# Performance work log

Measured on AMD Instinct MI355X. Metric: run time of the kernel, lower is better.

Reference implementation:

```python
import jax, jax.numpy as jnp
import numpy as np

B, T, IN, H, OUT = 4096, 512, 4, 64, 1


def setup_inputs() -> dict:
    key = jax.random.key(0)
    ks = jax.random.split(key, 12)
    s_in = 1.0 / np.sqrt(H)
    u = lambda k, shape: jax.random.uniform(k, shape, jnp.float32, -s_in, s_in)
    return {
        "x": jax.random.normal(ks[0], (B, T, IN), jnp.float32),
        "W_ih0": u(ks[1], (4 * H, IN)),
        "W_hh0": u(ks[2], (4 * H, H)),
        "b_ih0": u(ks[3], (4 * H,)),
        "b_hh0": u(ks[4], (4 * H,)),
        "W_ih1": u(ks[5], (4 * H, H)),
        "W_hh1": u(ks[6], (4 * H, H)),
        "b_ih1": u(ks[7], (4 * H,)),
        "b_hh1": u(ks[8], (4 * H,)),
        "W_fc": u(ks[9], (OUT, H)),
        "b_fc": u(ks[10], (OUT,)),
    }


def _lstm_layer(x_seq, W_ih, W_hh, b_ih, b_hh):
    # x_seq: [B, T, D]. PyTorch gate order: i, f, g, o.
    # Precompute input projection for all timesteps (one big GEMM).
    x_proj = jnp.einsum("btd,gd->btg", x_seq, W_ih) + b_ih + b_hh  # [B, T, 4H]
    x_proj = jnp.swapaxes(x_proj, 0, 1)  # [T, B, 4H]
    Bsz = x_seq.shape[0]
    h0 = jnp.zeros((Bsz, W_hh.shape[1]), x_seq.dtype)
    c0 = jnp.zeros_like(h0)

    def step(carry, xp):
        h, c = carry
        gates = xp + h @ W_hh.T  # [B, 4H]
        i, f, g, o = jnp.split(gates, 4, axis=-1)
        i = jax.nn.sigmoid(i)
        f = jax.nn.sigmoid(f)
        g = jnp.tanh(g)
        o = jax.nn.sigmoid(o)
        c_new = f * c + i * g
        h_new = o * jnp.tanh(c_new)
        return (h_new, c_new), h_new

    (hT, cT), h_seq = jax.lax.scan(step, (h0, c0), x_proj)
    return jnp.swapaxes(h_seq, 0, 1), hT  # [B, T, H], [B, H]


def reference(x, W_ih0, W_hh0, b_ih0, b_hh0, W_ih1, W_hh1, b_ih1, b_hh1, W_fc, b_fc):
    h1_seq, _ = _lstm_layer(x, W_ih0, W_hh0, b_ih0, b_hh0)
    _, h2_last = _lstm_layer(h1_seq, W_ih1, W_hh1, b_ih1, b_hh1)
    return h2_last @ W_fc.T + b_fc  # [B, 1]
```

## Files before the change

kernel.cpp:

```cpp
#include <hip/hip_runtime.h>

#define TSEQ 512
#define NTH  512

typedef __attribute__((ext_vector_type(8))) _Float16 half8;
typedef __attribute__((ext_vector_type(4))) float f32x4;
typedef __attribute__((ext_vector_type(4))) unsigned int u32x4;

__device__ __forceinline__ unsigned packF16x2(float a, float b) {
    _Float16 ha = (_Float16)a, hb = (_Float16)b;
    unsigned short ua = __builtin_bit_cast(unsigned short, ha);
    unsigned short ub = __builtin_bit_cast(unsigned short, hb);
    return (unsigned)ua | ((unsigned)ub << 16);
}
__device__ __forceinline__ half8 packA16s(const float w8[8], float s) {
    u32x4 W = { packF16x2(w8[0]*s, w8[1]*s), packF16x2(w8[2]*s, w8[3]*s),
                packF16x2(w8[4]*s, w8[5]*s), packF16x2(w8[6]*s, w8[7]*s) };
    return __builtin_bit_cast(half8, W);
}

#define MFMA(a, b, c) __builtin_amdgcn_mfma_f32_16x16x32_f16((a), (b), (c), 0, 0, 0)
#define LD128H(p) __builtin_bit_cast(half8, *(const u32x4*)(p))

__device__ __forceinline__ float act_fused(float ai, float af, float ag, float ao, float* c) {
    const float L2E2 = 2.88539008177792681472f;
    float ei = __builtin_amdgcn_exp2f(ai);
    float ef = __builtin_amdgcn_exp2f(af);
    float eg = __builtin_amdgcn_exp2f(ag);
    float eo = __builtin_amdgcn_exp2f(ao);
    float sf = __builtin_amdgcn_rcpf(1.0f + ef);
    float ig = (eg - 1.0f) * __builtin_amdgcn_rcpf((1.0f + ei) * (eg + 1.0f));
    float cn = fmaf(*c, sf, ig);
    *c = cn;
    float ec = __builtin_amdgcn_exp2f(cn * L2E2);
    return (ec - 1.0f) * __builtin_amdgcn_rcpf((1.0f + eo) * (ec + 1.0f));
}

__global__ __launch_bounds__(NTH, 1)
void lstm2_mfma(const float* __restrict__ x,
                const float* __restrict__ W_ih0, const float* __restrict__ W_hh0,
                const float* __restrict__ b_ih0, const float* __restrict__ b_hh0,
                const float* __restrict__ W_ih1, const float* __restrict__ W_hh1,
                const float* __restrict__ b_ih1, const float* __restrict__ b_hh1,
                const float* __restrict__ W_fc,  const float* __restrict__ b_fc,
                float* __restrict__ out)
{
    const int tid  = threadIdx.x;
    const int lane = tid & 63;
    const int wv   = tid >> 6;
    const int rl   = lane & 15;
    const int g    = lane >> 4;
    const int b0   = blockIdx.x * 16;

    const float NL2E = -1.44269504088896340736f;
    const float PL2E2 = 2.88539008177792681472f;

    __shared__ unsigned h0P0[512], h0P1[512];
    __shared__ unsigned h1P0[512], h1P1[512];
    __shared__ float fcl[64 * 17];

    for (int i2 = tid; i2 < 512; i2 += NTH) {
        h0P0[i2] = 0u; h0P1[i2] = 0u; h1P0[i2] = 0u; h1P1[i2] = 0u;
    }
    __syncthreads();

    const int offL = rl*32 + (((g + rl) & 7) << 2);
    const int offH = rl*32 + (((4 + g + rl) & 7) << 2);
    const int q0w  = 8*((wv & 3)) + 2*g;
    const int woff = rl*32 + ((((q0w >> 2) + rl) & 7) << 2) + (q0w & 3);

    if (wv < 4) {
        const int w = wv;
        half8 A0[4][2];
        half8 Ax[4];
        f32x4 bias4[4];
        #pragma unroll
        for (int G = 0; G < 4; ++G) {
            const float sc = (G == 2) ? PL2E2 : NL2E;
            const int row = 64*G + 16*w + rl;
            #pragma unroll
            for (int s = 0; s < 2; ++s) {
                float w8[8];
                const float* src = W_hh0 + row*64 + s*32 + g*8;
                #pragma unroll
                for (int e = 0; e < 8; ++e) w8[e] = src[e];
                A0[G][s] = packA16s(w8, sc);
            }
            {
                u32x4 ax = {0u, 0u, 0u, 0u};
                if (g == 0) {
                    ax.x = packF16x2(W_ih0[row*4+0]*sc, W_ih0[row*4+1]*sc);
                    ax.y = packF16x2(W_ih0[row*4+2]*sc, W_ih0[row*4+3]*sc);
                }
                Ax[G] = __builtin_bit_cast(half8, ax);
            }
            const int rb = 64*G + 16*w + 4*g;
            bias4[G].x = (b_ih0[rb+0] + b_hh0[rb+0]) * sc;
            bias4[G].y = (b_ih0[rb+1] + b_hh0[rb+1]) * sc;
            bias4[G].z = (b_ih0[rb+2] + b_hh0[rb+2]) * sc;
            bias4[G].w = (b_ih0[rb+3] + b_hh0[rb+3]) * sc;
        }
        float cst[4] = {0.f, 0.f, 0.f, 0.f};

        f32x4 xf = *(const f32x4*)(x + ((size_t)(b0 + rl) * TSEQ) * 4);
        unsigned bx0 = packF16x2(xf.x, xf.y);
        unsigned bx1 = packF16x2(xf.z, xf.w);

        auto body0 = [&](const unsigned* rP, unsigned* wP, int i) {
            if (i + 1 < TSEQ)
                xf = *(const f32x4*)(x + ((size_t)(b0 + rl) * TSEQ + (i + 1)) * 4);

            half8 B0 = LD128H(rP + offL);
            half8 B1 = LD128H(rP + offH);
            u32x4 tx = {0u, 0u, 0u, 0u};
            if (g == 0) { tx.x = bx0; tx.y = bx1; }
            half8 Bx = __builtin_bit_cast(half8, tx);

            f32x4 acc[4];
            __builtin_amdgcn_s_setprio(1);
            #pragma unroll
            for (int G = 0; G < 4; ++G) acc[G] = MFMA(Ax[G], Bx, bias4[G]);
            #pragma unroll
            for (int G = 0; G < 4; ++G) acc[G] = MFMA(A0[G][0], B0, acc[G]);
            #pragma unroll
            for (int G = 0; G < 4; ++G) acc[G] = MFMA(A0[G][1], B1, acc[G]);
            __builtin_amdgcn_s_setprio(0);

            float hv[4];
            #pragma unroll
            for (int j = 0; j < 4; ++j)
                hv[j] = act_fused(acc[0][j], acc[1][j], acc[2][j], acc[3][j], &cst[j]);

            bx0 = packF16x2(xf.x, xf.y);
            bx1 = packF16x2(xf.z, xf.w);

            *(uint2*)(wP + woff) = make_uint2(packF16x2(hv[0], hv[1]),
                                              packF16x2(hv[2], hv[3]));
        };

        for (int ii = 0; ii < 256; ++ii) {
            body0(h0P0, h0P1, 2*ii);     __syncthreads();
            body0(h0P1, h0P0, 2*ii + 1); __syncthreads();
        }
        __syncthreads();
        __syncthreads();
    } else {
        const int w = wv - 4;
        half8 A1[4][4];
        f32x4 bias4[4];
        #pragma unroll
        for (int G = 0; G < 4; ++G) {
            const float sc = (G == 2) ? PL2E2 : NL2E;
            const int row = 64*G + 16*w + rl;
            #pragma unroll
            for (int s = 0; s < 4; ++s) {
                float w8[8];
                const float* src = (s < 2) ? (W_ih1 + row*64 + s*32 + g*8)
                                           : (W_hh1 + row*64 + (s-2)*32 + g*8);
                #pragma unroll
                for (int e = 0; e < 8; ++e) w8[e] = src[e];
                A1[G][s] = packA16s(w8, sc);
            }
            const int rb = 64*G + 16*w + 4*g;
            bias4[G].x = (b_ih1[rb+0] + b_hh1[rb+0]) * sc;
            bias4[G].y = (b_ih1[rb+1] + b_hh1[rb+1]) * sc;
            bias4[G].z = (b_ih1[rb+2] + b_hh1[rb+2]) * sc;
            bias4[G].w = (b_ih1[rb+3] + b_hh1[rb+3]) * sc;
        }
        float cst[4] = {0.f, 0.f, 0.f, 0.f};
        const int u0 = 16*w + 4*g;

        half8 pB0 = {}, pB1 = {};

        auto body1 = [&](const unsigned* r1P,
                         unsigned* wP,
                         const unsigned* n0P,
                         bool wrFC) {
            half8 B2 = LD128H(r1P + offL);
            half8 B3 = LD128H(r1P + offH);

            f32x4 acc[4];
            __builtin_amdgcn_s_setprio(1);
            #pragma unroll
            for (int G = 0; G < 4; ++G) acc[G] = MFMA(A1[G][0], pB0, bias4[G]);
            #pragma unroll
            for (int G = 0; G < 4; ++G) acc[G] = MFMA(A1[G][1], pB1, acc[G]);
            #pragma unroll
            for (int G = 0; G < 4; ++G) acc[G] = MFMA(A1[G][2], B2, acc[G]);
            #pragma unroll
            for (int G = 0; G < 4; ++G) acc[G] = MFMA(A1[G][3], B3, acc[G]);
            __builtin_amdgcn_s_setprio(0);

            pB0 = LD128H(n0P + offL);
            pB1 = LD128H(n0P + offH);

            float hv[4];
            #pragma unroll
            for (int j = 0; j < 4; ++j)
                hv[j] = act_fused(acc[0][j], acc[1][j], acc[2][j], acc[3][j], &cst[j]);
            *(uint2*)(wP + woff) = make_uint2(packF16x2(hv[0], hv[1]),
                                              packF16x2(hv[2], hv[3]));
            if (wrFC) {
                #pragma unroll
                for (int j = 0; j < 4; ++j) fcl[(u0 + j)*17 + rl] = hv[j];
            }
        };

        __syncthreads();
        pB0 = LD128H(h0P1 + offL);
        pB1 = LD128H(h0P1 + offH);
        __syncthreads();
        for (int ii = 0; ii < 256; ++ii) {
            body1(h1P0, h1P1, h0P0, false);     __syncthreads();
            body1(h1P1, h1P0, h0P1, ii == 255); __syncthreads();
        }
    }

    if (tid < 16) {
        float acc = b_fc[0];
        #pragma unroll 16
        for (int u = 0; u < 64; ++u) acc += fcl[u*17 + tid] * W_fc[u];
        out[b0 + tid] = acc;
    }
}

extern "C" void kernel_launch(void* const* d_in, const int* in_sizes, int n_in,
                              void* d_out, int out_size, void* d_ws, size_t ws_size,
                              hipStream_t stream) {
    const float* x     = (const float*)d_in[0];
    const float* W_ih0 = (const float*)d_in[1];
    const float* W_hh0 = (const float*)d_in[2];
    const float* b_ih0 = (const float*)d_in[3];
    const float* b_hh0 = (const float*)d_in[4];
    const float* W_ih1 = (const float*)d_in[5];
    const float* W_hh1 = (const float*)d_in[6];
    const float* b_ih1 = (const float*)d_in[7];
    const float* b_hh1 = (const float*)d_in[8];
    const float* W_fc  = (const float*)d_in[9];
    const float* b_fc  = (const float*)d_in[10];
    float* out = (float*)d_out;

    dim3 grid(4096 / 16), block(NTH);
    hipLaunchKernelGGL(lstm2_mfma, grid, block, 0, stream,
                       x, W_ih0, W_hh0, b_ih0, b_hh0,
                       W_ih1, W_hh1, b_ih1, b_hh1, W_fc, b_fc, out);
}
```

Measured before the change: 341.7 us.

## Halve batch tile per block and give each wave two hidden-unit tiles

Blocks now handle 8 batch rows with 256 threads (two waves per layer) instead of 16 rows with 512 threads, and the grid doubles. Each wave keeps two 16-row weight tiles per gate and issues twice as many MFMAs per step. The 16 MFMA columns carry duplicated batch rows, and each lane selects the accumulator tile that matches its half. The aim is to cut per-block synchronization scope and spread the recurrence across more blocks. In exchange, MFMA work per batch element doubles, the serial MFMA chain per step gets longer, and register use for weights rises.

```diff
diff --git a/kernel.cpp b/kernel.cpp
--- a/kernel.cpp
+++ b/kernel.cpp
@@ -1,7 +1,8 @@
 #include <hip/hip_runtime.h>
 
 #define TSEQ 512
-#define NTH  512
+#define NTH  256
+#define BT   8
 
 typedef __attribute__((ext_vector_type(8))) _Float16 half8;
 typedef __attribute__((ext_vector_type(4))) float f32x4;
@@ -50,65 +51,68 @@
     const int wv   = tid >> 6;
     const int rl   = lane & 15;
     const int g    = lane >> 4;
-    const int b0   = blockIdx.x * 16;
-
-    const float NL2E = -1.44269504088896340736f;
-    const float PL2E2 = 2.88539008177792681472f;
-
-    __shared__ unsigned h0P0[512], h0P1[512];
-    __shared__ unsigned h1P0[512], h1P1[512];
-    __shared__ float fcl[64 * 17];
-
-    for (int i2 = tid; i2 < 512; i2 += NTH) {
+    const int n    = rl & 7;
+    const int T    = rl >> 3;
+    const int b0   = blockIdx.x * BT;
+    const int w    = wv & 1;
+
+    const float NL2E  = -1.44269504088896340736f;
+    const float PL2E2 =  2.88539008177792681472f;
+
+    __shared__ unsigned h0P0[256], h0P1[256];
+    __shared__ unsigned h1P0[256], h1P1[256];
+    __shared__ float fcl[64 * 9];
+
+    for (int i2 = tid; i2 < 256; i2 += NTH) {
         h0P0[i2] = 0u; h0P1[i2] = 0u; h1P0[i2] = 0u; h1P1[i2] = 0u;
     }
     __syncthreads();
 
-    const int offL = rl*32 + (((g + rl) & 7) << 2);
-    const int offH = rl*32 + (((4 + g + rl) & 7) << 2);
-    const int q0w  = 8*((wv & 3)) + 2*g;
-    const int woff = rl*32 + ((((q0w >> 2) + rl) & 7) << 2) + (q0w & 3);
-
-    if (wv < 4) {
-        const int w = wv;
-        half8 A0[4][2];
-        half8 Ax[4];
-        f32x4 bias4[4];
+    const int offL = n*32 + (((g + n) & 7) << 2);
+    const int offH = n*32 + (((4 + g + n) & 7) << 2);
+    const int q0w  = 16*w + 8*T + 2*g;
+    const int woff = n*32 + ((((q0w >> 2) + n) & 7) << 2) + (q0w & 3);
+
+    if (wv < 2) {
+        half8 A0[4][2][2];
+        half8 Ax[4][2];
+        f32x4 bias4[4][2];
         #pragma unroll
         for (int G = 0; G < 4; ++G) {
             const float sc = (G == 2) ? PL2E2 : NL2E;
-            const int row = 64*G + 16*w + rl;
-            #pragma unroll
-            for (int s = 0; s < 2; ++s) {
-                float w8[8];
-                const float* src = W_hh0 + row*64 + s*32 + g*8;
+            #pragma unroll
+            for (int Tt = 0; Tt < 2; ++Tt) {
+                const int row = 64*G + 32*w + 16*Tt + rl;
                 #pragma unroll
-                for (int e = 0; e < 8; ++e) w8[e] = src[e];
-                A0[G][s] = packA16s(w8, sc);
-            }
-            {
+                for (int s = 0; s < 2; ++s) {
+                    float w8[8];
+                    const float* src = W_hh0 + row*64 + s*32 + g*8;
+                    #pragma unroll
+                    for (int e = 0; e < 8; ++e) w8[e] = src[e];
+                    A0[G][s][Tt] = packA16s(w8, sc);
+                }
                 u32x4 ax = {0u, 0u, 0u, 0u};
                 if (g == 0) {
                     ax.x = packF16x2(W_ih0[row*4+0]*sc, W_ih0[row*4+1]*sc);
                     ax.y = packF16x2(W_ih0[row*4+2]*sc, W_ih0[row*4+3]*sc);
                 }
-                Ax[G] = __builtin_bit_cast(half8, ax);
+                Ax[G][Tt] = __builtin_bit_cast(half8, ax);
+                const int rb = 64*G + 32*w + 16*Tt + 4*g;
+                bias4[G][Tt].x = (b_ih0[rb+0] + b_hh0[rb+0]) * sc;
+                bias4[G][Tt].y = (b_ih0[rb+1] + b_hh0[rb+1]) * sc;
+                bias4[G][Tt].z = (b_ih0[rb+2] + b_hh0[rb+2]) * sc;
+                bias4[G][Tt].w = (b_ih0[rb+3] + b_hh0[rb+3]) * sc;
             }
-            const int rb = 64*G + 16*w + 4*g;
-            bias4[G].x = (b_ih0[rb+0] + b_hh0[rb+0]) * sc;
-            bias4[G].y = (b_ih0[rb+1] + b_hh0[rb+1]) * sc;
-            bias4[G].z = (b_ih0[rb+2] + b_hh0[rb+2]) * sc;
-            bias4[G].w = (b_ih0[rb+3] + b_hh0[rb+3]) * sc;
         }
         float cst[4] = {0.f, 0.f, 0.f, 0.f};
 
-        f32x4 xf = *(const f32x4*)(x + ((size_t)(b0 + rl) * TSEQ) * 4);
+        f32x4 xf = *(const f32x4*)(x + ((size_t)(b0 + n) * TSEQ) * 4);
         unsigned bx0 = packF16x2(xf.x, xf.y);
         unsigned bx1 = packF16x2(xf.z, xf.w);
 
         auto body0 = [&](const unsigned* rP, unsigned* wP, int i) {
             if (i + 1 < TSEQ)
-                xf = *(const f32x4*)(x + ((size_t)(b0 + rl) * TSEQ + (i + 1)) * 4);
+                xf = *(const f32x4*)(x + ((size_t)(b0 + n) * TSEQ + (i + 1)) * 4);
 
             half8 B0 = LD128H(rP + offL);
             half8 B1 = LD128H(rP + offH);
@@ -116,20 +120,30 @@
             if (g == 0) { tx.x = bx0; tx.y = bx1; }
             half8 Bx = __builtin_bit_cast(half8, tx);
 
-            f32x4 acc[4];
+            f32x4 acc[2][4];
             __builtin_amdgcn_s_setprio(1);
             #pragma unroll
-            for (int G = 0; G < 4; ++G) acc[G] = MFMA(Ax[G], Bx, bias4[G]);
-            #pragma unroll
-            for (int G = 0; G < 4; ++G) acc[G] = MFMA(A0[G][0], B0, acc[G]);
-            #pragma unroll
-            for (int G = 0; G < 4; ++G) acc[G] = MFMA(A0[G][1], B1, acc[G]);
+            for (int G = 0; G < 4; ++G) acc[0][G] = MFMA(Ax[G][0], Bx, bias4[G][0]);
+            #pragma unroll
+            for (int G = 0; G < 4; ++G) acc[1][G] = MFMA(Ax[G][1], Bx, bias4[G][1]);
+            #pragma unroll
+            for (int G = 0; G < 4; ++G) acc[0][G] = MFMA(A0[G][0][0], B0, acc[0][G]);
+            #pragma unroll
+            for (int G = 0; G < 4; ++G) acc[1][G] = MFMA(A0[G][0][1], B0, acc[1][G]);
+            #pragma unroll
+            for (int G = 0; G < 4; ++G) acc[0][G] = MFMA(A0[G][1][0], B1, acc[0][G]);
+            #pragma unroll
+            for (int G = 0; G < 4; ++G) acc[1][G] = MFMA(A0[G][1][1], B1, acc[1][G]);
             __builtin_amdgcn_s_setprio(0);
 
+            f32x4 s0 = T ? acc[1][0] : acc[0][0];
+            f32x4 s1 = T ? acc[1][1] : acc[0][1];
+            f32x4 s2 = T ? acc[1][2] : acc[0][2];
+            f32x4 s3 = T ? acc[1][3] : acc[0][3];
             float hv[4];
             #pragma unroll
             for (int j = 0; j < 4; ++j)
-                hv[j] = act_fused(acc[0][j], acc[1][j], acc[2][j], acc[3][j], &cst[j]);
+                hv[j] = act_fused(s0[j], s1[j], s2[j], s3[j], &cst[j]);
 
             bx0 = packF16x2(xf.x, xf.y);
             bx1 = packF16x2(xf.z, xf.w);
@@ -145,64 +159,76 @@
         __syncthreads();
         __syncthreads();
     } else {
-        const int w = wv - 4;
-        half8 A1[4][4];
-        f32x4 bias4[4];
+        half8 A1[4][4][2];
+        f32x4 bias4[4][2];
         #pragma unroll
         for (int G = 0; G < 4; ++G) {
             const float sc = (G == 2) ? PL2E2 : NL2E;
-            const int row = 64*G + 16*w + rl;
-            #pragma unroll
-            for (int s = 0; s < 4; ++s) {
-                float w8[8];
-                const float* src = (s < 2) ? (W_ih1 + row*64 + s*32 + g*8)
-                                           : (W_hh1 + row*64 + (s-2)*32 + g*8);
+            #pragma unroll
+            for (int Tt = 0; Tt < 2; ++Tt) {
+                const int row = 64*G + 32*w + 16*Tt + rl;
                 #pragma unroll
-                for (int e = 0; e < 8; ++e) w8[e] = src[e];
-                A1[G][s] = packA16s(w8, sc);
+                for (int s = 0; s < 4; ++s) {
+                    float w8[8];
+                    const float* src = (s < 2) ? (W_ih1 + row*64 + s*32 + g*8)
+                                               : (W_hh1 + row*64 + (s-2)*32 + g*8);
+                    #pragma unroll
+                    for (int e = 0; e < 8; ++e) w8[e] = src[e];
+                    A1[G][s][Tt] = packA16s(w8, sc);
+                }
+                const int rb = 64*G + 32*w + 16*Tt + 4*g;
+                bias4[G][Tt].x = (b_ih1[rb+0] + b_hh1[rb+0]) * sc;
+                bias4[G][Tt].y = (b_ih1[rb+1] + b_hh1[rb+1]) * sc;
+                bias4[G][Tt].z = (b_ih1[rb+2] + b_hh1[rb+2]) * sc;
+                bias4[G][Tt].w = (b_ih1[rb+3] + b_hh1[rb+3]) * sc;
             }
-            const int rb = 64*G + 16*w + 4*g;
-            bias4[G].x = (b_ih1[rb+0] + b_hh1[rb+0]) * sc;
-            bias4[G].y = (b_ih1[rb+1] + b_hh1[rb+1]) * sc;
-            bias4[G].z = (b_ih1[rb+2] + b_hh1[rb+2]) * sc;
-            bias4[G].w = (b_ih1[rb+3] + b_hh1[rb+3]) * sc;
         }
         float cst[4] = {0.f, 0.f, 0.f, 0.f};
-        const int u0 = 16*w + 4*g;
+        const int u0 = 32*w + 16*T + 4*g;
 
         half8 pB0 = {}, pB1 = {};
 
-        auto body1 = [&](const unsigned* r1P,
-                         unsigned* wP,
-                         const unsigned* n0P,
-                         bool wrFC) {
+        auto body1 = [&](const unsigned* r1P, unsigned* wP,
+                         const unsigned* n0P, bool wrFC) {
             half8 B2 = LD128H(r1P + offL);
             half8 B3 = LD128H(r1P + offH);
 
-            f32x4 acc[4];
+            f32x4 acc[2][4];
             __builtin_amdgcn_s_setprio(1);
             #pragma unroll
-            for (int G = 0; G < 4; ++G) acc[G] = MFMA(A1[G][0], pB0, bias4[G]);
-            #pragma unroll
-            for (int G = 0; G < 4; ++G) acc[G] = MFMA(A1[G][1], pB1, acc[G]);
-            #pragma unroll
-            for (int G = 0; G < 4; ++G) acc[G] = MFMA(A1[G][2], B2, acc[G]);
-            #pragma unroll
-            for (int G = 0; G < 4; ++G) acc[G] = MFMA(A1[G][3], B3, acc[G]);
+            for (int G = 0; G < 4; ++G) acc[0][G] = MFMA(A1[G][0][0], pB0, bias4[G][0]);
+            #pragma unroll
+            for (int G = 0; G < 4; ++G) acc[1][G] = MFMA(A1[G][0][1], pB0, bias4[G][1]);
+            #pragma unroll
+            for (int G = 0; G < 4; ++G) acc[0][G] = MFMA(A1[G][1][0], pB1, acc[0][G]);
+            #pragma unroll
+            for (int G = 0; G < 4; ++G) acc[1][G] = MFMA(A1[G][1][1], pB1, acc[1][G]);
+            #pragma unroll
+            for (int G = 0; G < 4; ++G) acc[0][G] = MFMA(A1[G][2][0], B2, acc[0][G]);
+            #pragma unroll
+            for (int G = 0; G < 4; ++G) acc[1][G] = MFMA(A1[G][2][1], B2, acc[1][G]);
+            #pragma unroll
+            for (int G = 0; G < 4; ++G) acc[0][G] = MFMA(A1[G][3][0], B3, acc[0][G]);
+            #pragma unroll
+            for (int G = 0; G < 4; ++G) acc[1][G] = MFMA(A1[G][3][1], B3, acc[1][G]);
             __builtin_amdgcn_s_setprio(0);
 
             pB0 = LD128H(n0P + offL);
             pB1 = LD128H(n0P + offH);
 
+            f32x4 s0 = T ? acc[1][0] : acc[0][0];
+            f32x4 s1 = T ? acc[1][1] : acc[0][1];
+            f32x4 s2 = T ? acc[1][2] : acc[0][2];
+            f32x4 s3 = T ? acc[1][3] : acc[0][3];
             float hv[4];
             #pragma unroll
             for (int j = 0; j < 4; ++j)
-                hv[j] = act_fused(acc[0][j], acc[1][j], acc[2][j], acc[3][j], &cst[j]);
+                hv[j] = act_fused(s0[j], s1[j], s2[j], s3[j], &cst[j]);
             *(uint2*)(wP + woff) = make_uint2(packF16x2(hv[0], hv[1]),
                                               packF16x2(hv[2], hv[3]));
             if (wrFC) {
                 #pragma unroll
-                for (int j = 0; j < 4; ++j) fcl[(u0 + j)*17 + rl] = hv[j];
+                for (int j = 0; j < 4; ++j) fcl[(u0 + j)*9 + n] = hv[j];
             }
         };
 
@@ -216,10 +242,10 @@
         }
     }
 
-    if (tid < 16) {
+    if (tid < BT) {
         float acc = b_fc[0];
         #pragma unroll 16
-        for (int u = 0; u < 64; ++u) acc += fcl[u*17 + tid] * W_fc[u];
+        for (int u = 0; u < 64; ++u) acc += fcl[u*9 + tid] * W_fc[u];
         out[b0 + tid] = acc;
     }
 }
@@ -240,7 +266,7 @@
     const float* b_fc  = (const float*)d_in[10];
     float* out = (float*)d_out;
 
-    dim3 grid(4096 / 16), block(NTH);
+    dim3 grid(4096 / BT), block(NTH);
     hipLaunchKernelGGL(lstm2_mfma, grid, block, 0, stream,
                        x, W_ih0, W_hh0, b_ih0, b_hh0,
                        W_ih1, W_hh1, b_ih1, b_hh1, W_fc, b_fc, out);
```

Measured after the change: 667.7 us. +95.4%, slower.

## Split each LSTM step into MFMA and activation phases interleaved across layers

Applied to the files above, without the earlier changes.

Each timestep is split into two phases separated by barriers. While layer 0 runs its MFMAs, layer 1 runs its activations, and the reverse in the next phase, so the two wave groups use the matrix and vector units at different times instead of contending. Layer 1 now keeps a single h buffer in shared memory. The cost is twice as many __syncthreads per timestep, which may outweigh the gain from the overlap.

```diff
diff --git a/kernel.cpp b/kernel.cpp
--- a/kernel.cpp
+++ b/kernel.cpp
@@ -52,15 +52,15 @@
     const int g    = lane >> 4;
     const int b0   = blockIdx.x * 16;
 
-    const float NL2E = -1.44269504088896340736f;
-    const float PL2E2 = 2.88539008177792681472f;
+    const float NL2E  = -1.44269504088896340736f;
+    const float PL2E2 =  2.88539008177792681472f;
 
     __shared__ unsigned h0P0[512], h0P1[512];
-    __shared__ unsigned h1P0[512], h1P1[512];
+    __shared__ unsigned h1P[512];
     __shared__ float fcl[64 * 17];
 
     for (int i2 = tid; i2 < 512; i2 += NTH) {
-        h0P0[i2] = 0u; h0P1[i2] = 0u; h1P0[i2] = 0u; h1P1[i2] = 0u;
+        h0P0[i2] = 0u; h0P1[i2] = 0u; h1P[i2] = 0u;
     }
     __syncthreads();
 
@@ -101,22 +101,20 @@
             bias4[G].w = (b_ih0[rb+3] + b_hh0[rb+3]) * sc;
         }
         float cst[4] = {0.f, 0.f, 0.f, 0.f};
+        f32x4 acc[4];
 
         f32x4 xf = *(const f32x4*)(x + ((size_t)(b0 + rl) * TSEQ) * 4);
         unsigned bx0 = packF16x2(xf.x, xf.y);
         unsigned bx1 = packF16x2(xf.z, xf.w);
 
-        auto body0 = [&](const unsigned* rP, unsigned* wP, int i) {
+        auto ph1 = [&](const unsigned* rP, int i) {
             if (i + 1 < TSEQ)
                 xf = *(const f32x4*)(x + ((size_t)(b0 + rl) * TSEQ + (i + 1)) * 4);
-
             half8 B0 = LD128H(rP + offL);
             half8 B1 = LD128H(rP + offH);
             u32x4 tx = {0u, 0u, 0u, 0u};
             if (g == 0) { tx.x = bx0; tx.y = bx1; }
             half8 Bx = __builtin_bit_cast(half8, tx);
-
-            f32x4 acc[4];
             __builtin_amdgcn_s_setprio(1);
             #pragma unroll
             for (int G = 0; G < 4; ++G) acc[G] = MFMA(Ax[G], Bx, bias4[G]);
@@ -125,25 +123,29 @@
             #pragma unroll
             for (int G = 0; G < 4; ++G) acc[G] = MFMA(A0[G][1], B1, acc[G]);
             __builtin_amdgcn_s_setprio(0);
-
+        };
+        auto ph2 = [&](unsigned* wP) {
             float hv[4];
             #pragma unroll
             for (int j = 0; j < 4; ++j)
                 hv[j] = act_fused(acc[0][j], acc[1][j], acc[2][j], acc[3][j], &cst[j]);
-
             bx0 = packF16x2(xf.x, xf.y);
             bx1 = packF16x2(xf.z, xf.w);
-
             *(uint2*)(wP + woff) = make_uint2(packF16x2(hv[0], hv[1]),
                                               packF16x2(hv[2], hv[3]));
         };
 
-        for (int ii = 0; ii < 256; ++ii) {
-            body0(h0P0, h0P1, 2*ii);     __syncthreads();
-            body0(h0P1, h0P0, 2*ii + 1); __syncthreads();
-        }
-        __syncthreads();
-        __syncthreads();
+        for (int ii = 0; ii <= 256; ++ii) {
+            const int i0 = 2*ii, i1 = 2*ii + 1;
+            if (i0 < TSEQ) ph1(h0P0, i0);
+            __syncthreads();
+            if (i0 < TSEQ) ph2(h0P1);
+            __syncthreads();
+            if (i1 < TSEQ) ph1(h0P1, i1);
+            __syncthreads();
+            if (i1 < TSEQ) ph2(h0P0);
+            __syncthreads();
+        }
     } else {
         const int w = wv - 4;
         half8 A1[4][4];
@@ -169,50 +171,54 @@
         }
         float cst[4] = {0.f, 0.f, 0.f, 0.f};
         const int u0 = 16*w + 4*g;
-
+        f32x4 acc[4];
         half8 pB0 = {}, pB1 = {};
 
-        auto body1 = [&](const unsigned* r1P,
-                         unsigned* wP,
-                         const unsigned* n0P,
-                         bool wrFC) {
-            half8 B2 = LD128H(r1P + offL);
-            half8 B3 = LD128H(r1P + offH);
-
-            f32x4 acc[4];
-            __builtin_amdgcn_s_setprio(1);
-            #pragma unroll
-            for (int G = 0; G < 4; ++G) acc[G] = MFMA(A1[G][0], pB0, bias4[G]);
-            #pragma unroll
-            for (int G = 0; G < 4; ++G) acc[G] = MFMA(A1[G][1], pB1, acc[G]);
-            #pragma unroll
-            for (int G = 0; G < 4; ++G) acc[G] = MFMA(A1[G][2], B2, acc[G]);
-            #pragma unroll
-            for (int G = 0; G < 4; ++G) acc[G] = MFMA(A1[G][3], B3, acc[G]);
-            __builtin_amdgcn_s_setprio(0);
-
-            pB0 = LD128H(n0P + offL);
-            pB1 = LD128H(n0P + offH);
-
-            float hv[4];
-            #pragma unroll
-            for (int j = 0; j < 4; ++j)
-                hv[j] = act_fused(acc[0][j], acc[1][j], acc[2][j], acc[3][j], &cst[j]);
-            *(uint2*)(wP + woff) = make_uint2(packF16x2(hv[0], hv[1]),
-                                              packF16x2(hv[2], hv[3]));
-            if (wrFC) {
-                #pragma unroll
-                for (int j = 0; j < 4; ++j) fcl[(u0 + j)*17 + rl] = hv[j];
-            }
-        };
-
-        __syncthreads();
-        pB0 = LD128H(h0P1 + offL);
-        pB1 = LD128H(h0P1 + offH);
-        __syncthreads();
-        for (int ii = 0; ii < 256; ++ii) {
-            body1(h1P0, h1P1, h0P0, false);     __syncthreads();
-            body1(h1P1, h1P0, h0P1, ii == 255); __syncthreads();
+        auto ph1 = [&](const unsigned* n0P, int i) {
+            if (i >= 2) {
+                float hv[4];
+                #pragma unroll
+                for (int j = 0; j < 4; ++j)
+                    hv[j] = act_fused(acc[0][j], acc[1][j], acc[2][j], acc[3][j], &cst[j]);
+                *(uint2*)(h1P + woff) = make_uint2(packF16x2(hv[0], hv[1]),
+                                                   packF16x2(hv[2], hv[3]));
+                if (i == TSEQ + 1) {
+                    #pragma unroll
+                    for (int j = 0; j < 4; ++j) fcl[(u0 + j)*17 + rl] = hv[j];
+                }
+            }
+            if (i >= 1 && i <= TSEQ) {
+                pB0 = LD128H(n0P + offL);
+                pB1 = LD128H(n0P + offH);
+            }
+        };
+        auto ph2 = [&](int i) {
+            if (i >= 1 && i <= TSEQ) {
+                half8 B2 = LD128H(h1P + offL);
+                half8 B3 = LD128H(h1P + offH);
+                __builtin_amdgcn_s_setprio(1);
+                #pragma unroll
+                for (int G = 0; G < 4; ++G) acc[G] = MFMA(A1[G][0], pB0, bias4[G]);
+                #pragma unroll
+                for (int G = 0; G < 4; ++G) acc[G] = MFMA(A1[G][1], pB1, acc[G]);
+                #pragma unroll
+                for (int G = 0; G < 4; ++G) acc[G] = MFMA(A1[G][2], B2, acc[G]);
+                #pragma unroll
+                for (int G = 0; G < 4; ++G) acc[G] = MFMA(A1[G][3], B3, acc[G]);
+                __builtin_amdgcn_s_setprio(0);
+            }
+        };
+
+        for (int ii = 0; ii <= 256; ++ii) {
+            const int i0 = 2*ii, i1 = 2*ii + 1;
+            ph1(h0P0, i0);
+            __syncthreads();
+            ph2(i0);
+            __syncthreads();
+            ph1(h0P1, i1);
+            __syncthreads();
+            ph2(i1);
+            __syncthreads();
         }
     }
 
```

New measurement: 363.2 us. +6.3%, slower.

## Halve batch per block to 8 and split activations across MFMA column halves

Applied to the files above, without the earlier changes.

Each block now handles 8 batch rows instead of 16, which doubles the grid to 512 blocks and allows two blocks per CU via launch bounds. The 16 MFMA columns now hold 8 batch rows duplicated across two halves. Each lane evaluates only 2 of its 4 accumulator outputs, so per-lane transcendental work on the serial recurrence drops by half. The cost is that the MFMA work is duplicated, and twice as many blocks each repeat the weight setup.

```diff
diff --git a/kernel.cpp b/kernel.cpp
--- a/kernel.cpp
+++ b/kernel.cpp
@@ -2,6 +2,7 @@
 
 #define TSEQ 512
 #define NTH  512
+#define BT   8
 
 typedef __attribute__((ext_vector_type(8))) _Float16 half8;
 typedef __attribute__((ext_vector_type(4))) float f32x4;
@@ -36,7 +37,7 @@
     return (ec - 1.0f) * __builtin_amdgcn_rcpf((1.0f + eo) * (ec + 1.0f));
 }
 
-__global__ __launch_bounds__(NTH, 1)
+__global__ __launch_bounds__(NTH, 2)
 void lstm2_mfma(const float* __restrict__ x,
                 const float* __restrict__ W_ih0, const float* __restrict__ W_hh0,
                 const float* __restrict__ b_ih0, const float* __restrict__ b_hh0,
@@ -50,24 +51,26 @@
     const int wv   = tid >> 6;
     const int rl   = lane & 15;
     const int g    = lane >> 4;
-    const int b0   = blockIdx.x * 16;
-
-    const float NL2E = -1.44269504088896340736f;
-    const float PL2E2 = 2.88539008177792681472f;
-
-    __shared__ unsigned h0P0[512], h0P1[512];
-    __shared__ unsigned h1P0[512], h1P1[512];
-    __shared__ float fcl[64 * 17];
-
-    for (int i2 = tid; i2 < 512; i2 += NTH) {
+    const int n    = rl & 7;
+    const int T    = rl >> 3;
+    const int b0   = blockIdx.x * BT;
+
+    const float NL2E  = -1.44269504088896340736f;
+    const float PL2E2 =  2.88539008177792681472f;
+
+    __shared__ unsigned h0P0[256], h0P1[256];
+    __shared__ unsigned h1P0[256], h1P1[256];
+    __shared__ float fcl[64 * 9];
+
+    for (int i2 = tid; i2 < 256; i2 += NTH) {
         h0P0[i2] = 0u; h0P1[i2] = 0u; h1P0[i2] = 0u; h1P1[i2] = 0u;
     }
     __syncthreads();
 
-    const int offL = rl*32 + (((g + rl) & 7) << 2);
-    const int offH = rl*32 + (((4 + g + rl) & 7) << 2);
-    const int q0w  = 8*((wv & 3)) + 2*g;
-    const int woff = rl*32 + ((((q0w >> 2) + rl) & 7) << 2) + (q0w & 3);
+    const int offL = n*32 + (((g + n) & 7) << 2);
+    const int offH = n*32 + (((4 + g + n) & 7) << 2);
+    const int q    = 8*((wv & 3)) + 2*g + T;
+    const int woff = n*32 + ((((q >> 2) + n) & 7) << 2) + (q & 3);
 
     if (wv < 4) {
         const int w = wv;
@@ -100,15 +103,15 @@
             bias4[G].z = (b_ih0[rb+2] + b_hh0[rb+2]) * sc;
             bias4[G].w = (b_ih0[rb+3] + b_hh0[rb+3]) * sc;
         }
-        float cst[4] = {0.f, 0.f, 0.f, 0.f};
-
-        f32x4 xf = *(const f32x4*)(x + ((size_t)(b0 + rl) * TSEQ) * 4);
+        float cst[2] = {0.f, 0.f};
+
+        f32x4 xf = *(const f32x4*)(x + ((size_t)(b0 + n) * TSEQ) * 4);
         unsigned bx0 = packF16x2(xf.x, xf.y);
         unsigned bx1 = packF16x2(xf.z, xf.w);
 
         auto body0 = [&](const unsigned* rP, unsigned* wP, int i) {
             if (i + 1 < TSEQ)
-                xf = *(const f32x4*)(x + ((size_t)(b0 + rl) * TSEQ + (i + 1)) * 4);
+                xf = *(const f32x4*)(x + ((size_t)(b0 + n) * TSEQ + (i + 1)) * 4);
 
             half8 B0 = LD128H(rP + offL);
             half8 B1 = LD128H(rP + offH);
@@ -126,16 +129,19 @@
             for (int G = 0; G < 4; ++G) acc[G] = MFMA(A0[G][1], B1, acc[G]);
             __builtin_amdgcn_s_setprio(0);
 
-            float hv[4];
-            #pragma unroll
-            for (int j = 0; j < 4; ++j)
-                hv[j] = act_fused(acc[0][j], acc[1][j], acc[2][j], acc[3][j], &cst[j]);
+            float s0[4], s1[4];
+            #pragma unroll
+            for (int G = 0; G < 4; ++G) {
+                s0[G] = T ? acc[G].z : acc[G].x;
+                s1[G] = T ? acc[G].w : acc[G].y;
+            }
+            float hv0 = act_fused(s0[0], s0[1], s0[2], s0[3], &cst[0]);
+            float hv1 = act_fused(s1[0], s1[1], s1[2], s1[3], &cst[1]);
 
             bx0 = packF16x2(xf.x, xf.y);
             bx1 = packF16x2(xf.z, xf.w);
 
-            *(uint2*)(wP + woff) = make_uint2(packF16x2(hv[0], hv[1]),
-                                              packF16x2(hv[2], hv[3]));
+            wP[woff] = packF16x2(hv0, hv1);
         };
 
         for (int ii = 0; ii < 256; ++ii) {
@@ -167,15 +173,13 @@
             bias4[G].z = (b_ih1[rb+2] + b_hh1[rb+2]) * sc;
             bias4[G].w = (b_ih1[rb+3] + b_hh1[rb+3]) * sc;
         }
-        float cst[4] = {0.f, 0.f, 0.f, 0.f};
-        const int u0 = 16*w + 4*g;
+        float cst[2] = {0.f, 0.f};
+        const int u0 = 16*w + 4*g + 2*T;
 
         half8 pB0 = {}, pB1 = {};
 
-        auto body1 = [&](const unsigned* r1P,
-                         unsigned* wP,
-                         const unsigned* n0P,
-                         bool wrFC) {
+        auto body1 = [&](const unsigned* r1P, unsigned* wP,
+                         const unsigned* n0P, bool wrFC) {
             half8 B2 = LD128H(r1P + offL);
             half8 B3 = LD128H(r1P + offH);
 
@@ -194,15 +198,18 @@
             pB0 = LD128H(n0P + offL);
             pB1 = LD128H(n0P + offH);
 
-            float hv[4];
-            #pragma unroll
-            for (int j = 0; j < 4; ++j)
-                hv[j] = act_fused(acc[0][j], acc[1][j], acc[2][j], acc[3][j], &cst[j]);
-            *(uint2*)(wP + woff) = make_uint2(packF16x2(hv[0], hv[1]),
-                                              packF16x2(hv[2], hv[3]));
+            float s0[4], s1[4];
+            #pragma unroll
+            for (int G = 0; G < 4; ++G) {
+                s0[G] = T ? acc[G].z : acc[G].x;
+                s1[G] = T ? acc[G].w : acc[G].y;
+            }
+            float hv0 = act_fused(s0[0], s0[1], s0[2], s0[3], &cst[0]);
+            float hv1 = act_fused(s1[0], s1[1], s1[2], s1[3], &cst[1]);
+            wP[woff] = packF16x2(hv0, hv1);
             if (wrFC) {
-                #pragma unroll
-                for (int j = 0; j < 4; ++j) fcl[(u0 + j)*17 + rl] = hv[j];
+                fcl[(u0 + 0)*9 + n] = hv0;
+                fcl[(u0 + 1)*9 + n] = hv1;
             }
         };
 
@@ -216,10 +223,10 @@
         }
     }
 
-    if (tid < 16) {
+    if (tid < BT) {
         float acc = b_fc[0];
         #pragma unroll 16
-        for (int u = 0; u < 64; ++u) acc += fcl[u*17 + tid] * W_fc[u];
+        for (int u = 0; u < 64; ++u) acc += fcl[u*9 + tid] * W_fc[u];
         out[b0 + tid] = acc;
     }
 }
@@ -240,7 +247,7 @@
     const float* b_fc  = (const float*)d_in[10];
     float* out = (float*)d_out;
 
-    dim3 grid(4096 / 16), block(NTH);
+    dim3 grid(4096 / BT), block(NTH);
     hipLaunchKernelGGL(lstm2_mfma, grid, block, 0, stream,
                        x, W_ih0, W_hh0, b_ih0, b_hh0,
                        W_ih1, W_hh1, b_ih1, b_hh1, W_fc, b_fc, out);
```

Result: slower. 540.2 us (+58.1%).
